# Optimization experiments

Hardware: AMD Instinct MI355X
Metric: run time of the kernel (lower is better)

Reference implementation:

```python
import jax, jax.numpy as jnp
import numpy as np

H = 64            # hidden_dim
N_NODES = 100000
N_EDGES = 2000000
IN_DIM = 2 * H + 2  # src_emb || dst_emb || src_fiedler || dst_fiedler


def setup_inputs() -> dict:
    key = jax.random.key(0)
    ks = jax.random.split(key, 10)
    node_embeddings = jax.random.normal(ks[0], (N_NODES, H), dtype=jnp.float32)
    edge_index = jax.random.randint(ks[1], (2, N_EDGES), 0, N_NODES, dtype=jnp.int64)
    fiedler_vector = jax.random.normal(ks[2], (N_NODES,), dtype=jnp.float32)
    # MLP scorer params: Linear(130,64)+ReLU, Linear(64,64)+ReLU, Linear(64,1)
    def lin(k, fan_in, fan_out):
        bound = 1.0 / np.sqrt(fan_in)
        kw, kb = jax.random.split(k)
        W = jax.random.uniform(kw, (fan_in, fan_out), jnp.float32, -bound, bound)
        b = jax.random.uniform(kb, (fan_out,), jnp.float32, -bound, bound)
        return W, b
    W1, b1 = lin(ks[3], IN_DIM, H)
    W2, b2 = lin(ks[4], H, H)
    W3, b3 = lin(ks[5], H, 1)
    return {
        "node_embeddings": node_embeddings,
        "fiedler_vector": fiedler_vector,
        "W1": W1, "b1": b1, "W2": W2, "b2": b2, "W3": W3, "b3": b3,
        "edge_index": edge_index,
        "num_nodes": N_NODES,
    }


def reference(node_embeddings, fiedler_vector, W1, b1, W2, b2, W3, b3, edge_index, num_nodes):
    src, dst = edge_index[0], edge_index[1]
    # Gather + concat edge features: [E, 2H+2]
    feats = jnp.concatenate(
        [
            node_embeddings[src],               # [E, H]
            node_embeddings[dst],               # [E, H]
            fiedler_vector[src][:, None],        # [E, 1]
            fiedler_vector[dst][:, None],        # [E, 1]
        ],
        axis=-1,
    )
    # Edge scorer MLP (Dropout is identity in eval mode)
    h = jax.nn.relu(feats @ W1 + b1)
    h = jax.nn.relu(h @ W2 + b2)
    edge_scores = (h @ W3 + b3)[:, 0]  # [E]
    return edge_scores
```

## Files before the change

kernel.cpp:

```cpp
#include <hip/hip_runtime.h>


#define HD 64

typedef __attribute__((ext_vector_type(8))) _Float16 half8;
typedef __attribute__((ext_vector_type(4))) _Float16 half4;
typedef __attribute__((ext_vector_type(2))) _Float16 half2v;
typedef __attribute__((ext_vector_type(2))) __fp16  fp16x2;
typedef __attribute__((ext_vector_type(8))) short  short8;
typedef __attribute__((ext_vector_type(2))) short  short2v;
typedef __attribute__((ext_vector_type(8))) float  float8;
typedef __attribute__((ext_vector_type(4))) float  f32x4;

__device__ __forceinline__ half8 relu_h8(half8 x) {
    short8 b = __builtin_bit_cast(short8, x);
    short8 m = b >> 15;
    b = b & ~m;
    return __builtin_bit_cast(half8, b);
}
__device__ __forceinline__ half2v relu_h2(half2v x) {
    short2v b = __builtin_bit_cast(short2v, x);
    short2v m = b >> 15;
    b = b & ~m;
    return __builtin_bit_cast(half2v, b);
}
__device__ __forceinline__ half2v pkrtz(float a, float b) {
    return __builtin_bit_cast(half2v, __builtin_amdgcn_cvt_pkrtz(a, b));
}
__device__ __forceinline__ float fdot2f(half2v a, half2v b, float c) {
    return __builtin_amdgcn_fdot2(__builtin_bit_cast(fp16x2, a),
                                  __builtin_bit_cast(fp16x2, b), c, false);
}

__global__ __launch_bounds__(256) void precompute_uv(
    const float* __restrict__ emb, const float* __restrict__ fied,
    const float* __restrict__ W1, const float* __restrict__ b1,
    _Float16* __restrict__ u, _Float16* __restrict__ v,
    int n_nodes, int ntiles)
{
    const int lane = threadIdx.x & 63;
    const int q = lane >> 4;
    const int c = lane & 15;
    const int wid = blockIdx.x * (blockDim.x >> 6) + (threadIdx.x >> 6);
    const int nw  = gridDim.x * (blockDim.x >> 6);

    half8 Au[4][2], Av[4][2];
    #pragma unroll
    for (int t = 0; t < 4; ++t)
        #pragma unroll
        for (int ks = 0; ks < 2; ++ks)
            #pragma unroll
            for (int j = 0; j < 8; ++j) {
                int k = ks * 32 + q * 8 + j;
                Au[t][ks][j] = (_Float16)W1[k * HD + t * 16 + c];
                Av[t][ks][j] = (_Float16)W1[(64 + k) * HD + t * 16 + c];
            }
    f32x4 b1q[4], wsq[4], wdq[4];
    #pragma unroll
    for (int t = 0; t < 4; ++t) {
        b1q[t] = *(const f32x4*)(b1 + t * 16 + q * 4);
        wsq[t] = *(const f32x4*)(W1 + 128 * HD + t * 16 + q * 4);
        wdq[t] = *(const f32x4*)(W1 + 129 * HD + t * 16 + q * 4);
    }

    for (int tile = wid; tile < ntiles; tile += nw) {
        const int n0 = tile * 16;
        const int n  = n0 + c;
        int na = n; if (na >= n_nodes) na = n_nodes - 1;
        const float* rp = emb + (size_t)na * HD + q * 8;
        float8 a0 = *(const float8*)rp;
        float8 a1 = *(const float8*)(rp + 32);
        half8 B0 = __builtin_convertvector(a0, half8);
        half8 B1 = __builtin_convertvector(a1, half8);

        f32x4 aU[4] = {}, aV[4] = {};
        #pragma unroll
        for (int t = 0; t < 4; ++t) {
            aU[t] = __builtin_amdgcn_mfma_f32_16x16x32_f16(Au[t][0], B0, aU[t], 0, 0, 0);
            aU[t] = __builtin_amdgcn_mfma_f32_16x16x32_f16(Au[t][1], B1, aU[t], 0, 0, 0);
            aV[t] = __builtin_amdgcn_mfma_f32_16x16x32_f16(Av[t][0], B0, aV[t], 0, 0, 0);
            aV[t] = __builtin_amdgcn_mfma_f32_16x16x32_f16(Av[t][1], B1, aV[t], 0, 0, 0);
        }

        const float fv = fied[na];
        const bool ok = (n < n_nodes);
        #pragma unroll
        for (int t = 0; t < 4; ++t) {
            half4 hu, hv;
            #pragma unroll
            for (int r = 0; r < 4; ++r) {
                hu[r] = (_Float16)(aU[t][r] + b1q[t][r] + fv * wsq[t][r]);
                hv[r] = (_Float16)(aV[t][r] + fv * wdq[t][r]);
            }
            if (ok) {
                *(half4*)(u + (size_t)n * HD + t * 16 + q * 4) = hu;
                *(half4*)(v + (size_t)n * HD + t * 16 + q * 4) = hv;
            }
        }
    }
}

__global__ __launch_bounds__(256) void edge_mlp(
    const _Float16* __restrict__ u, const _Float16* __restrict__ v,
    const int* __restrict__ src, const int* __restrict__ dst,
    const float* __restrict__ W2, const float* __restrict__ b2,
    const float* __restrict__ W3, const float* __restrict__ b3,
    float* __restrict__ out, int E, int ntiles)
{
    const int lane = threadIdx.x & 63;
    const int q = lane >> 4;
    const int c = lane & 15;
    const int wid = blockIdx.x * (blockDim.x >> 6) + (threadIdx.x >> 6);
    const int nw  = gridDim.x * (blockDim.x >> 6);

    half8 Af[4][2];
    #pragma unroll
    for (int t = 0; t < 4; ++t)
        #pragma unroll
        for (int ks = 0; ks < 2; ++ks)
            #pragma unroll
            for (int j = 0; j < 8; ++j) {
                int k = ks * 32 + q * 8 + j;
                Af[t][ks][j] = (_Float16)W2[k * HD + t * 16 + c];
            }
    half2v b2p[4][2], w3p[4][2];
    #pragma unroll
    for (int t = 0; t < 4; ++t) {
        int f = t * 16 + q * 4;
        b2p[t][0] = half2v{(_Float16)b2[f],     (_Float16)b2[f + 1]};
        b2p[t][1] = half2v{(_Float16)b2[f + 2], (_Float16)b2[f + 3]};
        w3p[t][0] = half2v{(_Float16)W3[f],     (_Float16)W3[f + 1]};
        w3p[t][1] = half2v{(_Float16)W3[f + 2], (_Float16)W3[f + 3]};
    }
    const float b3v = b3[0];

    auto eid = [&](int tile) {
        int t = tile; if (t >= ntiles) t = ntiles - 1;
        int e = t * 16 + c; if (e >= E) e = E - 1;
        return e;
    };
    auto issue = [&](int s, int d, half8& Ua, half8& Ub, half8& Va, half8& Vb) {
        const half8* up = (const half8*)(u + (unsigned)s * HD + q * 8);
        const half8* vp = (const half8*)(v + (unsigned)d * HD + q * 8);
        Ua = up[0]; Ub = up[4]; Va = vp[0]; Vb = vp[4];
    };
    auto compute_store = [&](int tile, half8 Ua, half8 Ub, half8 Va, half8 Vb) {
        half8 B0 = relu_h8(Ua + Va);
        half8 B1 = relu_h8(Ub + Vb);
        float p = 0.f;
        #pragma unroll
        for (int t = 0; t < 4; ++t) {
            f32x4 acc = {};
            acc = __builtin_amdgcn_mfma_f32_16x16x32_f16(Af[t][0], B0, acc, 0, 0, 0);
            acc = __builtin_amdgcn_mfma_f32_16x16x32_f16(Af[t][1], B1, acc, 0, 0, 0);
            half2v h0 = relu_h2(pkrtz(acc[0], acc[1]) + b2p[t][0]);
            half2v h1 = relu_h2(pkrtz(acc[2], acc[3]) + b2p[t][1]);
            p = fdot2f(h0, w3p[t][0], p);
            p = fdot2f(h1, w3p[t][1], p);
        }
        p += __shfl_xor(p, 16, 64);
        p += __shfl_xor(p, 32, 64);
        if (q == 0) {
            int e = tile * 16 + c;
            if (e < E) out[e] = p + b3v;
        }
    };

    const int stride = nw * 4;
    const int base0  = wid * 4;
    if (base0 >= ntiles) return;

    half8 U0a,U0b,V0a,V0b, U1a,U1b,V1a,V1b, U2a,U2b,V2a,V2b, U3a,U3b,V3a,V3b;
    {
        int e0 = eid(base0), e1 = eid(base0+1), e2 = eid(base0+2), e3 = eid(base0+3);
        issue(src[e0], dst[e0], U0a, U0b, V0a, V0b);
        issue(src[e1], dst[e1], U1a, U1b, V1a, V1b);
        issue(src[e2], dst[e2], U2a, U2b, V2a, V2b);
        issue(src[e3], dst[e3], U3a, U3b, V3a, V3b);
    }
    int sc0, dc0, sc1, dc1, sc2, dc2, sc3, dc3;
    {
        int f0 = eid(base0+stride),   f1 = eid(base0+stride+1),
            f2 = eid(base0+stride+2), f3 = eid(base0+stride+3);
        sc0 = src[f0]; dc0 = dst[f0]; sc1 = src[f1]; dc1 = dst[f1];
        sc2 = src[f2]; dc2 = dst[f2]; sc3 = src[f3]; dc3 = dst[f3];
    }

    for (int base = base0; base < ntiles; base += stride) {
        const int g0 = eid(base + 2*stride),     g1 = eid(base + 2*stride + 1),
                  g2 = eid(base + 2*stride + 2), g3 = eid(base + 2*stride + 3);
        const int sn0 = src[g0], dn0 = dst[g0];
        const int sn1 = src[g1], dn1 = dst[g1];
        const int sn2 = src[g2], dn2 = dst[g2];
        const int sn3 = src[g3], dn3 = dst[g3];

        compute_store(base,     U0a, U0b, V0a, V0b);
        issue(sc0, dc0, U0a, U0b, V0a, V0b);
        compute_store(base + 1, U1a, U1b, V1a, V1b);
        issue(sc1, dc1, U1a, U1b, V1a, V1b);
        compute_store(base + 2, U2a, U2b, V2a, V2b);
        issue(sc2, dc2, U2a, U2b, V2a, V2b);
        compute_store(base + 3, U3a, U3b, V3a, V3b);
        issue(sc3, dc3, U3a, U3b, V3a, V3b);

        sc0 = sn0; dc0 = dn0; sc1 = sn1; dc1 = dn1;
        sc2 = sn2; dc2 = dn2; sc3 = sn3; dc3 = dn3;
    }
}

extern "C" void kernel_launch(void* const* d_in, const int* in_sizes, int n_in,
                              void* d_out, int out_size, void* d_ws, size_t ws_size,
                              hipStream_t stream) {
    const float* emb  = (const float*)d_in[0];
    const float* fied = (const float*)d_in[1];
    const float* W1   = (const float*)d_in[2];
    const float* b1   = (const float*)d_in[3];
    const float* W2   = (const float*)d_in[4];
    const float* b2   = (const float*)d_in[5];
    const float* W3   = (const float*)d_in[6];
    const float* b3   = (const float*)d_in[7];
    const int*   eidx = (const int*)d_in[8];

    const int n_nodes = in_sizes[1];
    const int E       = in_sizes[8] / 2;
    const int* srcp = eidx;
    const int* dstp = eidx + E;

    _Float16* u = (_Float16*)d_ws;
    _Float16* v = u + (size_t)n_nodes * HD;

    const int ntilesN = (n_nodes + 15) / 16;
    precompute_uv<<<1024, 256, 0, stream>>>(emb, fied, W1, b1, u, v,
                                            n_nodes, ntilesN);

    const int ntilesE = (E + 15) / 16;
    edge_mlp<<<2048, 256, 0, stream>>>(u, v, srcp, dstp, W2, b2, W3, b3,
                                       (float*)d_out, E, ntilesE);
}
```

Before: 183.7 us.

## Bucket edges by source node before edge MLP to improve gather locality

Adds a counting-sort pipeline (histogram, per-wave prefix assignment, atomic scatter) that groups edges by source node, then runs the edge MLP over the reordered src/dst lists and writes each score back to its original edge id. The aim is better cache reuse on the u-row gathers, since consecutive edges now share source nodes. It also cuts the main loop's prefetch depth from 4 tiles to 2 to make room for the extra edge-id register. The cost is three extra kernels plus two memsets, a full extra read/write pass over the edge arrays, scattered output stores, and the sort only runs if the workspace is large enough.

```diff
diff --git a/kernel.cpp b/kernel.cpp
--- a/kernel.cpp
+++ b/kernel.cpp
@@ -100,9 +100,55 @@
     }
 }
 
+__global__ __launch_bounds__(256) void hist_k(
+    const int* __restrict__ src, int* __restrict__ cnt, int E)
+{
+    int i  = blockIdx.x * blockDim.x + threadIdx.x;
+    int st = gridDim.x * blockDim.x;
+    for (; i < E; i += st) atomicAdd(&cnt[src[i]], 1);
+}
+
+__global__ __launch_bounds__(256) void assign_k(
+    const int* __restrict__ cnt, int* __restrict__ curs,
+    int* __restrict__ gcnt, int nn)
+{
+    const int lane = threadIdx.x & 63;
+    const int w    = (blockIdx.x * blockDim.x + threadIdx.x) >> 6;
+    const int bin  = w * 64 + lane;
+    int x = (bin < nn) ? cnt[bin] : 0;
+    int inc = x;
+    #pragma unroll
+    for (int off = 1; off < 64; off <<= 1) {
+        int t = __shfl_up(inc, off, 64);
+        if (lane >= off) inc += t;
+    }
+    int ex = inc - x;
+    int base = 0;
+    if (lane == 63) base = atomicAdd(gcnt, inc);
+    base = __shfl(base, 63, 64);
+    if (bin < nn) curs[bin] = base + ex;
+}
+
+__global__ __launch_bounds__(256) void scatter_k(
+    const int* __restrict__ src, const int* __restrict__ dst,
+    int* __restrict__ curs, int* __restrict__ ssrc,
+    int* __restrict__ sdst, int* __restrict__ seid, int E)
+{
+    int i  = blockIdx.x * blockDim.x + threadIdx.x;
+    int st = gridDim.x * blockDim.x;
+    for (; i < E; i += st) {
+        int s = src[i];
+        int p = atomicAdd(&curs[s], 1);
+        ssrc[p] = s;
+        sdst[p] = dst[i];
+        seid[p] = i;
+    }
+}
+
 __global__ __launch_bounds__(256) void edge_mlp(
     const _Float16* __restrict__ u, const _Float16* __restrict__ v,
     const int* __restrict__ src, const int* __restrict__ dst,
+    const int* __restrict__ seid,
     const float* __restrict__ W2, const float* __restrict__ b2,
     const float* __restrict__ W3, const float* __restrict__ b3,
     float* __restrict__ out, int E, int ntiles)
@@ -139,12 +185,17 @@
         int e = t * 16 + c; if (e >= E) e = E - 1;
         return e;
     };
+    auto ldidx = [&](int tile, int& s, int& d, int& g) {
+        int e = eid(tile);
+        s = src[e]; d = dst[e];
+        g = seid ? seid[e] : e;
+    };
     auto issue = [&](int s, int d, half8& Ua, half8& Ub, half8& Va, half8& Vb) {
         const half8* up = (const half8*)(u + (unsigned)s * HD + q * 8);
         const half8* vp = (const half8*)(v + (unsigned)d * HD + q * 8);
         Ua = up[0]; Ub = up[4]; Va = vp[0]; Vb = vp[4];
     };
-    auto compute_store = [&](int tile, half8 Ua, half8 Ub, half8 Va, half8 Vb) {
+    auto compute_store = [&](int tile, int g, half8 Ua, half8 Ub, half8 Va, half8 Vb) {
         half8 B0 = relu_h8(Ua + Va);
         half8 B1 = relu_h8(Ub + Vb);
         float p = 0.f;
@@ -162,49 +213,38 @@
         p += __shfl_xor(p, 32, 64);
         if (q == 0) {
             int e = tile * 16 + c;
-            if (e < E) out[e] = p + b3v;
-        }
-    };
-
-    const int stride = nw * 4;
-    const int base0  = wid * 4;
+            if (e < E) out[g] = p + b3v;
+        }
+    };
+
+    const int stride = nw * 2;
+    const int base0  = wid * 2;
     if (base0 >= ntiles) return;
 
-    half8 U0a,U0b,V0a,V0b, U1a,U1b,V1a,V1b, U2a,U2b,V2a,V2b, U3a,U3b,V3a,V3b;
-    {
-        int e0 = eid(base0), e1 = eid(base0+1), e2 = eid(base0+2), e3 = eid(base0+3);
-        issue(src[e0], dst[e0], U0a, U0b, V0a, V0b);
-        issue(src[e1], dst[e1], U1a, U1b, V1a, V1b);
-        issue(src[e2], dst[e2], U2a, U2b, V2a, V2b);
-        issue(src[e3], dst[e3], U3a, U3b, V3a, V3b);
-    }
-    int sc0, dc0, sc1, dc1, sc2, dc2, sc3, dc3;
-    {
-        int f0 = eid(base0+stride),   f1 = eid(base0+stride+1),
-            f2 = eid(base0+stride+2), f3 = eid(base0+stride+3);
-        sc0 = src[f0]; dc0 = dst[f0]; sc1 = src[f1]; dc1 = dst[f1];
-        sc2 = src[f2]; dc2 = dst[f2]; sc3 = src[f3]; dc3 = dst[f3];
-    }
+    int s0, d0, g0, s1, d1, g1;
+    ldidx(base0, s0, d0, g0);
+    ldidx(base0 + 1, s1, d1, g1);
+    half8 U0a, U0b, V0a, V0b, U1a, U1b, V1a, V1b;
+    issue(s0, d0, U0a, U0b, V0a, V0b);
+    issue(s1, d1, U1a, U1b, V1a, V1b);
+    int sc0, dc0, gc0, sc1, dc1, gc1;
+    ldidx(base0 + stride,     sc0, dc0, gc0);
+    ldidx(base0 + stride + 1, sc1, dc1, gc1);
 
     for (int base = base0; base < ntiles; base += stride) {
-        const int g0 = eid(base + 2*stride),     g1 = eid(base + 2*stride + 1),
-                  g2 = eid(base + 2*stride + 2), g3 = eid(base + 2*stride + 3);
-        const int sn0 = src[g0], dn0 = dst[g0];
-        const int sn1 = src[g1], dn1 = dst[g1];
-        const int sn2 = src[g2], dn2 = dst[g2];
-        const int sn3 = src[g3], dn3 = dst[g3];
-
-        compute_store(base,     U0a, U0b, V0a, V0b);
+        int sn0, dn0, gn0, sn1, dn1, gn1;
+        ldidx(base + 2 * stride,     sn0, dn0, gn0);
+        ldidx(base + 2 * stride + 1, sn1, dn1, gn1);
+
+        compute_store(base, g0, U0a, U0b, V0a, V0b);
         issue(sc0, dc0, U0a, U0b, V0a, V0b);
-        compute_store(base + 1, U1a, U1b, V1a, V1b);
+        g0 = gc0;
+        compute_store(base + 1, g1, U1a, U1b, V1a, V1b);
         issue(sc1, dc1, U1a, U1b, V1a, V1b);
-        compute_store(base + 2, U2a, U2b, V2a, V2b);
-        issue(sc2, dc2, U2a, U2b, V2a, V2b);
-        compute_store(base + 3, U3a, U3b, V3a, V3b);
-        issue(sc3, dc3, U3a, U3b, V3a, V3b);
-
-        sc0 = sn0; dc0 = dn0; sc1 = sn1; dc1 = dn1;
-        sc2 = sn2; dc2 = dn2; sc3 = sn3; dc3 = dn3;
+        g1 = gc1;
+
+        sc0 = sn0; dc0 = dn0; gc0 = gn0;
+        sc1 = sn1; dc1 = dn1; gc1 = gn1;
     }
 }
 
@@ -221,19 +261,39 @@
     const float* b3   = (const float*)d_in[7];
     const int*   eidx = (const int*)d_in[8];
 
-    const int n_nodes = in_sizes[1];
-    const int E       = in_sizes[8] / 2;
+    const int nn = in_sizes[1];
+    const int E  = in_sizes[8] / 2;
     const int* srcp = eidx;
     const int* dstp = eidx + E;
 
-    _Float16* u = (_Float16*)d_ws;
-    _Float16* v = u + (size_t)n_nodes * HD;
-
-    const int ntilesN = (n_nodes + 15) / 16;
-    precompute_uv<<<1024, 256, 0, stream>>>(emb, fied, W1, b1, u, v,
-                                            n_nodes, ntilesN);
+    char* w = (char*)d_ws;
+    _Float16* u = (_Float16*)w;                       w += (size_t)nn * HD * 2;
+    _Float16* v = (_Float16*)w;                       w += (size_t)nn * HD * 2;
+    size_t base_need = (size_t)(w - (char*)d_ws);
+    int* cnt  = (int*)w;                              w += (size_t)nn * 4;
+    int* curs = (int*)w;                              w += (size_t)nn * 4;
+    int* gcnt = (int*)w;                              w += 64;
+    int* ssrc = (int*)w;                              w += (size_t)E * 4;
+    int* sdst = (int*)w;                              w += (size_t)E * 4;
+    int* sid  = (int*)w;                              w += (size_t)E * 4;
+    const bool do_sort = ((size_t)(w - (char*)d_ws) <= ws_size);
+    (void)base_need;
+
+    const int ntilesN = (nn + 15) / 16;
+    precompute_uv<<<1024, 256, 0, stream>>>(emb, fied, W1, b1, u, v, nn, ntilesN);
 
     const int ntilesE = (E + 15) / 16;
-    edge_mlp<<<2048, 256, 0, stream>>>(u, v, srcp, dstp, W2, b2, W3, b3,
-                                       (float*)d_out, E, ntilesE);
-}
+    if (do_sort) {
+        hipMemsetAsync(cnt, 0, (size_t)nn * 4, stream);
+        hipMemsetAsync(gcnt, 0, 4, stream);
+        hist_k<<<2048, 256, 0, stream>>>(srcp, cnt, E);
+        const int nwaves = (nn + 63) / 64;
+        assign_k<<<(nwaves + 3) / 4, 256, 0, stream>>>(cnt, curs, gcnt, nn);
+        scatter_k<<<2048, 256, 0, stream>>>(srcp, dstp, curs, ssrc, sdst, sid, E);
+        edge_mlp<<<2048, 256, 0, stream>>>(u, v, ssrc, sdst, sid, W2, b2, W3, b3,
+                                           (float*)d_out, E, ntilesE);
+    } else {
+        edge_mlp<<<2048, 256, 0, stream>>>(u, v, srcp, dstp, nullptr, W2, b2, W3, b3,
+                                           (float*)d_out, E, ntilesE);
+    }
+}
```

After: 388.8 us. +111.7%, slower.
